# Performance work log

Hardware: AMD Instinct MI355X
Metric: run time of the kernel (lower is better)

## Reference

```python
import jax, jax.numpy as jnp
import numpy as np

NUM_GROUPS = 131072
GROUP_SIZE = 3          # trigenic interaction queries (Dango)
HIDDEN = 128
NUM_HEADS = 4
HEAD_DIM = HIDDEN // NUM_HEADS
NUM_LAYERS = 2


def setup_inputs() -> dict:
    key = jax.random.key(0)
    ks = jax.random.split(key, 16)
    N = NUM_GROUPS * GROUP_SIZE
    H, L = HIDDEN, NUM_LAYERS
    s = 1.0 / np.sqrt(H)
    inp = {
        "gene_embeddings": jax.random.normal(ks[0], (N, H), dtype=jnp.float32),
        "batch": jnp.repeat(jnp.arange(NUM_GROUPS, dtype=jnp.int64), GROUP_SIZE),
        # static embedding Linear
        "Ws": jax.random.uniform(ks[1], (H, H), jnp.float32, -s, s),
        "bs": jnp.zeros((H,), jnp.float32),
        # per-layer attention projections, stacked over layers
        "Wq": jax.random.uniform(ks[2], (L, H, H), jnp.float32, -s, s),
        "bq": jnp.zeros((L, H), jnp.float32),
        "Wk": jax.random.uniform(ks[3], (L, H, H), jnp.float32, -s, s),
        "bk": jnp.zeros((L, H), jnp.float32),
        "Wv": jax.random.uniform(ks[4], (L, H, H), jnp.float32, -s, s),
        "bv": jnp.zeros((L, H), jnp.float32),
        "Wo": jax.random.uniform(ks[5], (L, H, H), jnp.float32, -s, s),
        "bo": jnp.zeros((L, H), jnp.float32),
        # ReZero params, init 0.01 as in module
        "beta": jnp.full((L,), 0.01, jnp.float32),
        # prediction layer (xavier_uniform)
        "Wp": jax.random.uniform(ks[6], (H, 1), jnp.float32, -np.sqrt(6.0 / (H + 1)), np.sqrt(6.0 / (H + 1))),
        "bp": jnp.zeros((1,), jnp.float32),
    }
    return inp


def _attention_layer(xg, Wq, bq, Wk, bk, Wv, bv, Wo, bo, beta):
    # xg: [G, S, H] block-diagonal groups; exclude-self masked MHA + ReZero.
    G, S, H = xg.shape
    q = (xg @ Wq + bq).reshape(G, S, NUM_HEADS, HEAD_DIM)
    k = (xg @ Wk + bk).reshape(G, S, NUM_HEADS, HEAD_DIM)
    v = (xg @ Wv + bv).reshape(G, S, NUM_HEADS, HEAD_DIM)
    scores = jnp.einsum("gqhd,gkhd->ghqk", q, k) / np.sqrt(HEAD_DIM)
    self_mask = jnp.eye(S, dtype=bool)  # exclude self-attention
    scores = jnp.where(self_mask, -jnp.inf, scores)
    attn = jax.nn.softmax(scores, axis=-1)
    attn = jnp.nan_to_num(attn, nan=0.0)  # torch.nan_to_num parity
    out = jnp.einsum("ghqk,gkhd->gqhd", attn, v).reshape(G, S, H)
    out = out @ Wo + bo
    return xg + beta * out  # ReZero residual (dropout: eval mode identity)


def reference(gene_embeddings, batch, Ws, bs, Wq, bq, Wk, bk, Wv, bv, Wo, bo, beta, Wp, bp):
    N, H = gene_embeddings.shape
    G = N // GROUP_SIZE
    static = jax.nn.relu(gene_embeddings @ Ws + bs)  # static embedding MLP
    dyn = gene_embeddings.reshape(G, GROUP_SIZE, H)
    for i in range(NUM_LAYERS):
        dyn = _attention_layer(dyn, Wq[i], bq[i], Wk[i], bk[i],
                               Wv[i], bv[i], Wo[i], bo[i], beta[i])
    dyn = dyn.reshape(N, H)
    diff_sq = (dyn - static) ** 2
    gene_scores = (diff_sq @ Wp + bp).squeeze(-1)  # [N]
    # scatter_mean over batch ids
    sums = jax.ops.segment_sum(gene_scores, batch, num_segments=G)
    cnts = jax.ops.segment_sum(jnp.ones_like(gene_scores), batch, num_segments=G)
    interaction_scores = sums / jnp.maximum(cnts, 1.0)
    return interaction_scores[:, None]  # [G, 1]
```

## Files before the change

### kernel.cpp

```cpp
#include <hip/hip_runtime.h>

#define NGROUPS 131072
#define H 128
#define SG 3
#define NHEADS 4
#define HD 32
#define GB 16
#define MR 48
#define NT 512
#define BP 136
#define NLAYERS 2

typedef unsigned short u16;
typedef __bf16 bf16x8 __attribute__((ext_vector_type(8)));
typedef float floatx4 __attribute__((ext_vector_type(4)));

__device__ __forceinline__ float bf2f(u16 u) {
  union { unsigned int i; float f; } c; c.i = ((unsigned int)u) << 16; return c.f;
}
__device__ __forceinline__ u16 f2bf(float f) {
  union { float f; unsigned int i; } c; c.f = f;
  unsigned int x = c.i;
  x += 0x7fffu + ((x >> 16) & 1u);
  return (u16)(x >> 16);
}

__global__ void wconv_kernel(const float* __restrict__ Ws, const float* __restrict__ Wq,
                             const float* __restrict__ Wk, const float* __restrict__ Wv,
                             const float* __restrict__ Wo, u16* __restrict__ wt) {
  int idx = blockIdx.x * 256 + threadIdx.x;
  int slot = idx >> 14;
  int rem = idx & 16383;
  int n = rem >> 7, k = rem & 127;
  const float* src;
  if (slot == 0) src = Ws;
  else {
    int l = (slot - 1) >> 2, t = (slot - 1) & 3;
    const float* base = (t == 0) ? Wq : (t == 1) ? Wk : (t == 2) ? Wv : Wo;
    src = base + l * (H * H);
  }
  wt[idx] = f2bf(src[k * H + n]);
}

__device__ __forceinline__ void load_af(const u16* __restrict__ buf, int m0, int q8,
                                        bf16x8 af[3][4]) {
#pragma unroll
  for (int rt = 0; rt < 3; rt++)
#pragma unroll
    for (int kk = 0; kk < 4; kk++)
      af[rt][kk] = *reinterpret_cast<const bf16x8*>(buf + (rt * 16 + m0) * BP + kk * 32 + q8);
}

__device__ __forceinline__ void mm_sub(const bf16x8 af[3][4], const u16* __restrict__ W,
                                       int col, int q8, floatx4 acc[3]) {
  bf16x8 b[4];
#pragma unroll
  for (int kk = 0; kk < 4; kk++)
    b[kk] = *reinterpret_cast<const bf16x8*>(W + col * H + kk * 32 + q8);
#pragma unroll
  for (int rt = 0; rt < 3; rt++)
    acc[rt] = (floatx4){0.f, 0.f, 0.f, 0.f};
#pragma unroll
  for (int kk = 0; kk < 4; kk++)
#pragma unroll
    for (int rt = 0; rt < 3; rt++)
      acc[rt] = __builtin_amdgcn_mfma_f32_16x16x32_bf16(af[rt][kk], b[kk], acc[rt], 0, 0, 0);
}

__device__ __forceinline__ void store_bf(u16* __restrict__ buf, const floatx4 acc[3],
                                         float bias, int col, int qi) {
#pragma unroll
  for (int rt = 0; rt < 3; rt++)
#pragma unroll
    for (int r = 0; r < 4; r++)
      buf[(rt * 16 + qi * 4 + r) * BP + col] = f2bf(acc[rt][r] + bias);
}

__global__ void __launch_bounds__(NT, 4)
dango_kernel(const float* __restrict__ x, const u16* __restrict__ wt,
             const float* __restrict__ bs, const float* __restrict__ bq,
             const float* __restrict__ bk, const float* __restrict__ bv,
             const float* __restrict__ bo, const float* __restrict__ beta,
             const float* __restrict__ Wp, const float* __restrict__ bp,
             float* __restrict__ out)
{
  __shared__ u16 xbf[MR][BP];
  __shared__ u16 qbuf[MR][BP];
  __shared__ u16 kbuf[MR][BP];
  __shared__ float attnw[GB][NHEADS][SG][2];
  __shared__ float rowsc[MR][9];

  const int tid = threadIdx.x;
  const int lane = tid & 63;
  const int wave = tid >> 6;
  const int m0 = lane & 15;
  const int qi = lane >> 4;
  const int q8 = qi << 3;
  const int col = wave * 16 + m0;
  const int row0 = blockIdx.x * MR;

  float xdyn[3][4];
#pragma unroll
  for (int rt = 0; rt < 3; rt++)
#pragma unroll
    for (int r = 0; r < 4; r++) {
      int row = rt * 16 + qi * 4 + r;
      float v = x[(size_t)(row0 + row) * H + col];
      xdyn[rt][r] = v;
      xbf[row][col] = f2bf(v);
    }
  __syncthreads();

  float stat[3][4];
  bf16x8 af[3][4];
  floatx4 acc[3];

  load_af(&xbf[0][0], m0, q8, af);
  __syncthreads();

  mm_sub(af, wt, col, q8, acc);
  {
    float b = bs[col];
#pragma unroll
    for (int rt = 0; rt < 3; rt++)
#pragma unroll
      for (int r = 0; r < 4; r++)
        stat[rt][r] = fmaxf(acc[rt][r] + b, 0.f);
  }
  mm_sub(af, wt + (size_t)1 * H * H, col, q8, acc);
  store_bf(&qbuf[0][0], acc, bq[col], col, qi);
  mm_sub(af, wt + (size_t)2 * H * H, col, q8, acc);
  store_bf(&kbuf[0][0], acc, bk[col], col, qi);
  mm_sub(af, wt + (size_t)3 * H * H, col, q8, acc);
  store_bf(&xbf[0][0], acc, bv[col], col, qi);
  __syncthreads();

  for (int l = 0; l < NLAYERS; l++) {
    if (tid < GB * NHEADS * SG) {
      int g = tid / (NHEADS * SG);
      int rem = tid % (NHEADS * SG);
      int h = rem / SG;
      int i = rem % SG;
      int j0 = (i == 0) ? 1 : 0;
      int j1 = (i == 2) ? 1 : 2;
      const u16* qp = &qbuf[g * 3 + i][h * HD];
      const u16* k0p = &kbuf[g * 3 + j0][h * HD];
      const u16* k1p = &kbuf[g * 3 + j1][h * HD];
      float s0 = 0.f, s1 = 0.f;
#pragma unroll
      for (int d = 0; d < HD; d++) {
        float qv = bf2f(qp[d]);
        s0 += qv * bf2f(k0p[d]);
        s1 += qv * bf2f(k1p[d]);
      }
      s0 *= 0.17677669529663687f;
      s1 *= 0.17677669529663687f;
      float mx = fmaxf(s0, s1);
      float e0 = __expf(s0 - mx), e1 = __expf(s1 - mx);
      float inv = 1.f / (e0 + e1);
      attnw[g][h][i][0] = e0 * inv;
      attnw[g][h][i][1] = e1 * inv;
    }
    __syncthreads();

    for (int ch = tid; ch < MR * 16; ch += NT) {
      int r = ch >> 4, c0 = (ch & 15) << 3;
      int g = r / 3, i = r - g * 3, h = c0 >> 5;
      int j0 = (i == 0) ? 1 : 0;
      int j1 = (i == 2) ? 1 : 2;
      float a0 = attnw[g][h][i][0], a1 = attnw[g][h][i][1];
      const u16* v0 = &xbf[g * 3 + j0][c0];
      const u16* v1 = &xbf[g * 3 + j1][c0];
#pragma unroll
      for (int d = 0; d < 8; d++)
        qbuf[r][c0 + d] = f2bf(a0 * bf2f(v0[d]) + a1 * bf2f(v1[d]));
    }
    __syncthreads();

    const u16* wo = wt + (size_t)(1 + l * 4 + 3) * H * H;
    const float betal = beta[l];
    load_af(&qbuf[0][0], m0, q8, af);
    mm_sub(af, wo, col, q8, acc);
    {
      float b = bo[l * H + col];
#pragma unroll
      for (int rt = 0; rt < 3; rt++)
#pragma unroll
        for (int r = 0; r < 4; r++) {
          float nv = xdyn[rt][r] + betal * (acc[rt][r] + b);
          xdyn[rt][r] = nv;
          xbf[(rt * 16 + qi * 4 + r)][col] = f2bf(nv);
        }
    }
    __syncthreads();

    if (l + 1 < NLAYERS) {
      const u16* wq = wt + (size_t)(1 + (l + 1) * 4 + 0) * H * H;
      const u16* wk = wt + (size_t)(1 + (l + 1) * 4 + 1) * H * H;
      const u16* wv = wt + (size_t)(1 + (l + 1) * 4 + 2) * H * H;
      load_af(&xbf[0][0], m0, q8, af);
      __syncthreads();
      mm_sub(af, wq, col, q8, acc);
      store_bf(&qbuf[0][0], acc, bq[(l + 1) * H + col], col, qi);
      mm_sub(af, wk, col, q8, acc);
      store_bf(&kbuf[0][0], acc, bk[(l + 1) * H + col], col, qi);
      mm_sub(af, wv, col, q8, acc);
      store_bf(&xbf[0][0], acc, bv[(l + 1) * H + col], col, qi);
      __syncthreads();
    }
  }

  const float wpc = Wp[col];
  float rv[3][4];
#pragma unroll
  for (int rt = 0; rt < 3; rt++)
#pragma unroll
    for (int r = 0; r < 4; r++) {
      float d = xdyn[rt][r] - stat[rt][r];
      rv[rt][r] = d * d * wpc;
    }
#pragma unroll
  for (int mask = 1; mask <= 8; mask <<= 1)
#pragma unroll
    for (int rt = 0; rt < 3; rt++)
#pragma unroll
      for (int r = 0; r < 4; r++)
        rv[rt][r] += __shfl_xor(rv[rt][r], mask, 64);
  if (m0 == 0) {
#pragma unroll
    for (int rt = 0; rt < 3; rt++)
#pragma unroll
      for (int r = 0; r < 4; r++)
        rowsc[rt * 16 + qi * 4 + r][wave] = rv[rt][r];
  }
  __syncthreads();
  if (tid < GB) {
    const float bpv = bp[0];
    float s = 0.f;
#pragma unroll
    for (int i = 0; i < SG; i++) {
      int row = tid * 3 + i;
#pragma unroll
      for (int w = 0; w < 8; w++) s += rowsc[row][w];
    }
    out[blockIdx.x * GB + tid] = s * (1.f / 3.f) + bpv;
  }
}

extern "C" void kernel_launch(void* const* d_in, const int* in_sizes, int n_in,
                              void* d_out, int out_size, void* d_ws, size_t ws_size,
                              hipStream_t stream) {
  const float* x    = (const float*)d_in[0];
  const float* Ws   = (const float*)d_in[2];
  const float* bs   = (const float*)d_in[3];
  const float* Wq   = (const float*)d_in[4];
  const float* bq   = (const float*)d_in[5];
  const float* Wk   = (const float*)d_in[6];
  const float* bk   = (const float*)d_in[7];
  const float* Wv   = (const float*)d_in[8];
  const float* bv   = (const float*)d_in[9];
  const float* Wo   = (const float*)d_in[10];
  const float* bo   = (const float*)d_in[11];
  const float* beta = (const float*)d_in[12];
  const float* Wp   = (const float*)d_in[13];
  const float* bp   = (const float*)d_in[14];
  float* out = (float*)d_out;
  u16* wt = (u16*)d_ws;

  wconv_kernel<<<576, 256, 0, stream>>>(Ws, Wq, Wk, Wv, Wo, wt);
  dango_kernel<<<NGROUPS / GB, NT, 0, stream>>>(x, wt, bs, bq, bk, bv, bo, beta, Wp, bp, out);
}
```

Baseline: 616.8 us.

## Transpose MFMA operands so each lane owns four contiguous columns, vectorize LDS traffic

Swaps the A and B roles in the projection MFMAs so the weight tile is the A operand and the activations are B. Each lane now holds four consecutive output columns of one row, which allows float4 global loads of x, packed bf16x2 stores to LDS, and a shorter shuffle reduction at the end. The attention score and value-mix loops read and write LDS as uint4 instead of scalar u16. A separate V buffer removes one barrier, and the static branch is kept as packed bf16 to reduce register pressure under a fixed 4-waves-per-EU bound. The cost is extra LDS and a small precision loss in the static path.

```diff
diff --git a/kernel.cpp b/kernel.cpp
--- a/kernel.cpp
+++ b/kernel.cpp
@@ -1,4 +1,5 @@
 #include <hip/hip_runtime.h>
+#include <hip/hip_bf16.h>
 
 #define NGROUPS 131072
 #define H 128
@@ -12,16 +13,23 @@
 #define NLAYERS 2
 
 typedef unsigned short u16;
+typedef unsigned int u32;
 typedef __bf16 bf16x8 __attribute__((ext_vector_type(8)));
 typedef float floatx4 __attribute__((ext_vector_type(4)));
 
-__device__ __forceinline__ float bf2f(u16 u) {
-  union { unsigned int i; float f; } c; c.i = ((unsigned int)u) << 16; return c.f;
+__device__ __forceinline__ float bf2f_lo(u32 u) {
+  union { u32 i; float f; } c; c.i = u << 16; return c.f;
+}
+__device__ __forceinline__ float bf2f_hi(u32 u) {
+  union { u32 i; float f; } c; c.i = u & 0xffff0000u; return c.f;
+}
+__device__ __forceinline__ u32 f2bf2(float a, float b) {
+  __hip_bfloat162 h = __float22bfloat162_rn(make_float2(a, b));
+  union { __hip_bfloat162 h; u32 u; } c; c.h = h; return c.u;
 }
 __device__ __forceinline__ u16 f2bf(float f) {
-  union { float f; unsigned int i; } c; c.f = f;
-  unsigned int x = c.i;
-  x += 0x7fffu + ((x >> 16) & 1u);
+  union { float f; u32 i; } c; c.f = f;
+  u32 x = c.i; x += 0x7fffu + ((x >> 16) & 1u);
   return (u16)(x >> 16);
 }
 
@@ -42,41 +50,44 @@
   wt[idx] = f2bf(src[k * H + n]);
 }
 
-__device__ __forceinline__ void load_af(const u16* __restrict__ buf, int m0, int q8,
-                                        bf16x8 af[3][4]) {
-#pragma unroll
-  for (int rt = 0; rt < 3; rt++)
+__device__ __forceinline__ void load_bfrag(const u16* __restrict__ buf, int m0, int qi,
+                                           bf16x8 bf[3][4]) {
+#pragma unroll
+  for (int nt = 0; nt < 3; nt++)
 #pragma unroll
     for (int kk = 0; kk < 4; kk++)
-      af[rt][kk] = *reinterpret_cast<const bf16x8*>(buf + (rt * 16 + m0) * BP + kk * 32 + q8);
-}
-
-__device__ __forceinline__ void mm_sub(const bf16x8 af[3][4], const u16* __restrict__ W,
-                                       int col, int q8, floatx4 acc[3]) {
-  bf16x8 b[4];
+      bf[nt][kk] = *reinterpret_cast<const bf16x8*>(buf + (nt * 16 + m0) * BP + kk * 32 + qi * 8);
+}
+
+__device__ __forceinline__ void proj(const bf16x8 bf[3][4], const u16* __restrict__ W,
+                                     int wrow, int qi, floatx4 acc[3]) {
+  bf16x8 a[4];
 #pragma unroll
   for (int kk = 0; kk < 4; kk++)
-    b[kk] = *reinterpret_cast<const bf16x8*>(W + col * H + kk * 32 + q8);
-#pragma unroll
-  for (int rt = 0; rt < 3; rt++)
-    acc[rt] = (floatx4){0.f, 0.f, 0.f, 0.f};
+    a[kk] = *reinterpret_cast<const bf16x8*>(W + wrow * H + kk * 32 + qi * 8);
+#pragma unroll
+  for (int nt = 0; nt < 3; nt++)
+    acc[nt] = (floatx4){0.f, 0.f, 0.f, 0.f};
 #pragma unroll
   for (int kk = 0; kk < 4; kk++)
 #pragma unroll
-    for (int rt = 0; rt < 3; rt++)
-      acc[rt] = __builtin_amdgcn_mfma_f32_16x16x32_bf16(af[rt][kk], b[kk], acc[rt], 0, 0, 0);
-}
-
-__device__ __forceinline__ void store_bf(u16* __restrict__ buf, const floatx4 acc[3],
-                                         float bias, int col, int qi) {
-#pragma unroll
-  for (int rt = 0; rt < 3; rt++)
-#pragma unroll
-    for (int r = 0; r < 4; r++)
-      buf[(rt * 16 + qi * 4 + r) * BP + col] = f2bf(acc[rt][r] + bias);
-}
-
-__global__ void __launch_bounds__(NT, 4)
+    for (int nt = 0; nt < 3; nt++)
+      acc[nt] = __builtin_amdgcn_mfma_f32_16x16x32_bf16(a[kk], bf[nt][kk], acc[nt], 0, 0, 0);
+}
+
+__device__ __forceinline__ void store_proj(u16* __restrict__ buf, const floatx4 acc[3],
+                                           float4 b4, int m0, int colb) {
+#pragma unroll
+  for (int nt = 0; nt < 3; nt++) {
+    uint2 pp;
+    pp.x = f2bf2(acc[nt][0] + b4.x, acc[nt][1] + b4.y);
+    pp.y = f2bf2(acc[nt][2] + b4.z, acc[nt][3] + b4.w);
+    *reinterpret_cast<uint2*>(buf + (nt * 16 + m0) * BP + colb) = pp;
+  }
+}
+
+__global__ void __launch_bounds__(NT)
+__attribute__((amdgpu_waves_per_eu(4, 4)))
 dango_kernel(const float* __restrict__ x, const u16* __restrict__ wt,
              const float* __restrict__ bs, const float* __restrict__ bq,
              const float* __restrict__ bk, const float* __restrict__ bv,
@@ -84,9 +95,10 @@
              const float* __restrict__ Wp, const float* __restrict__ bp,
              float* __restrict__ out)
 {
-  __shared__ u16 xbf[MR][BP];
-  __shared__ u16 qbuf[MR][BP];
-  __shared__ u16 kbuf[MR][BP];
+  __shared__ __align__(16) u16 xbf[MR][BP];
+  __shared__ __align__(16) u16 qbuf[MR][BP];
+  __shared__ __align__(16) u16 kbuf[MR][BP];
+  __shared__ __align__(16) u16 vbuf[MR][BP];
   __shared__ float attnw[GB][NHEADS][SG][2];
   __shared__ float rowsc[MR][9];
 
@@ -95,44 +107,44 @@
   const int wave = tid >> 6;
   const int m0 = lane & 15;
   const int qi = lane >> 4;
-  const int q8 = qi << 3;
-  const int col = wave * 16 + m0;
+  const int colb = wave * 16 + qi * 4;
+  const int wrow = wave * 16 + m0;
   const int row0 = blockIdx.x * MR;
 
   float xdyn[3][4];
-#pragma unroll
-  for (int rt = 0; rt < 3; rt++)
-#pragma unroll
-    for (int r = 0; r < 4; r++) {
-      int row = rt * 16 + qi * 4 + r;
-      float v = x[(size_t)(row0 + row) * H + col];
-      xdyn[rt][r] = v;
-      xbf[row][col] = f2bf(v);
-    }
+  u32 statpk[3][2];
+
+#pragma unroll
+  for (int nt = 0; nt < 3; nt++) {
+    int row = nt * 16 + m0;
+    float4 v = *reinterpret_cast<const float4*>(x + (size_t)(row0 + row) * H + colb);
+    xdyn[nt][0] = v.x; xdyn[nt][1] = v.y; xdyn[nt][2] = v.z; xdyn[nt][3] = v.w;
+    uint2 pp; pp.x = f2bf2(v.x, v.y); pp.y = f2bf2(v.z, v.w);
+    *reinterpret_cast<uint2*>(&xbf[row][colb]) = pp;
+  }
   __syncthreads();
 
-  float stat[3][4];
-  bf16x8 af[3][4];
   floatx4 acc[3];
-
-  load_af(&xbf[0][0], m0, q8, af);
-  __syncthreads();
-
-  mm_sub(af, wt, col, q8, acc);
   {
-    float b = bs[col];
-#pragma unroll
-    for (int rt = 0; rt < 3; rt++)
-#pragma unroll
-      for (int r = 0; r < 4; r++)
-        stat[rt][r] = fmaxf(acc[rt][r] + b, 0.f);
-  }
-  mm_sub(af, wt + (size_t)1 * H * H, col, q8, acc);
-  store_bf(&qbuf[0][0], acc, bq[col], col, qi);
-  mm_sub(af, wt + (size_t)2 * H * H, col, q8, acc);
-  store_bf(&kbuf[0][0], acc, bk[col], col, qi);
-  mm_sub(af, wt + (size_t)3 * H * H, col, q8, acc);
-  store_bf(&xbf[0][0], acc, bv[col], col, qi);
+    bf16x8 bf[3][4];
+    load_bfrag(&xbf[0][0], m0, qi, bf);
+
+    proj(bf, wt, wrow, qi, acc);
+    {
+      float4 b4 = *reinterpret_cast<const float4*>(bs + colb);
+#pragma unroll
+      for (int nt = 0; nt < 3; nt++) {
+        statpk[nt][0] = f2bf2(fmaxf(acc[nt][0] + b4.x, 0.f), fmaxf(acc[nt][1] + b4.y, 0.f));
+        statpk[nt][1] = f2bf2(fmaxf(acc[nt][2] + b4.z, 0.f), fmaxf(acc[nt][3] + b4.w, 0.f));
+      }
+    }
+    proj(bf, wt + 1 * H * H, wrow, qi, acc);
+    store_proj(&qbuf[0][0], acc, *reinterpret_cast<const float4*>(bq + colb), m0, colb);
+    proj(bf, wt + 2 * H * H, wrow, qi, acc);
+    store_proj(&kbuf[0][0], acc, *reinterpret_cast<const float4*>(bk + colb), m0, colb);
+    proj(bf, wt + 3 * H * H, wrow, qi, acc);
+    store_proj(&vbuf[0][0], acc, *reinterpret_cast<const float4*>(bv + colb), m0, colb);
+  }
   __syncthreads();
 
   for (int l = 0; l < NLAYERS; l++) {
@@ -143,15 +155,22 @@
       int i = rem % SG;
       int j0 = (i == 0) ? 1 : 0;
       int j1 = (i == 2) ? 1 : 2;
-      const u16* qp = &qbuf[g * 3 + i][h * HD];
-      const u16* k0p = &kbuf[g * 3 + j0][h * HD];
-      const u16* k1p = &kbuf[g * 3 + j1][h * HD];
+      const uint4* qp  = reinterpret_cast<const uint4*>(&qbuf[g * 3 + i][h * HD]);
+      const uint4* k0p = reinterpret_cast<const uint4*>(&kbuf[g * 3 + j0][h * HD]);
+      const uint4* k1p = reinterpret_cast<const uint4*>(&kbuf[g * 3 + j1][h * HD]);
       float s0 = 0.f, s1 = 0.f;
 #pragma unroll
-      for (int d = 0; d < HD; d++) {
-        float qv = bf2f(qp[d]);
-        s0 += qv * bf2f(k0p[d]);
-        s1 += qv * bf2f(k1p[d]);
+      for (int c = 0; c < 4; c++) {
+        uint4 qu = qp[c], u0 = k0p[c], u1 = k1p[c];
+        u32 qs[4] = {qu.x, qu.y, qu.z, qu.w};
+        u32 a0[4] = {u0.x, u0.y, u0.z, u0.w};
+        u32 a1[4] = {u1.x, u1.y, u1.z, u1.w};
+#pragma unroll
+        for (int e = 0; e < 4; e++) {
+          float ql = bf2f_lo(qs[e]), qh = bf2f_hi(qs[e]);
+          s0 += ql * bf2f_lo(a0[e]) + qh * bf2f_hi(a0[e]);
+          s1 += ql * bf2f_lo(a1[e]) + qh * bf2f_hi(a1[e]);
+        }
       }
       s0 *= 0.17677669529663687f;
       s1 *= 0.17677669529663687f;
@@ -169,73 +188,81 @@
       int j0 = (i == 0) ? 1 : 0;
       int j1 = (i == 2) ? 1 : 2;
       float a0 = attnw[g][h][i][0], a1 = attnw[g][h][i][1];
-      const u16* v0 = &xbf[g * 3 + j0][c0];
-      const u16* v1 = &xbf[g * 3 + j1][c0];
-#pragma unroll
-      for (int d = 0; d < 8; d++)
-        qbuf[r][c0 + d] = f2bf(a0 * bf2f(v0[d]) + a1 * bf2f(v1[d]));
+      uint4 v0 = *reinterpret_cast<const uint4*>(&vbuf[g * 3 + j0][c0]);
+      uint4 v1 = *reinterpret_cast<const uint4*>(&vbuf[g * 3 + j1][c0]);
+      u32 w0[4] = {v0.x, v0.y, v0.z, v0.w};
+      u32 w1[4] = {v1.x, v1.y, v1.z, v1.w};
+      u32 oo[4];
+#pragma unroll
+      for (int e = 0; e < 4; e++) {
+        float lo = a0 * bf2f_lo(w0[e]) + a1 * bf2f_lo(w1[e]);
+        float hi = a0 * bf2f_hi(w0[e]) + a1 * bf2f_hi(w1[e]);
+        oo[e] = f2bf2(lo, hi);
+      }
+      uint4 o; o.x = oo[0]; o.y = oo[1]; o.z = oo[2]; o.w = oo[3];
+      *reinterpret_cast<uint4*>(&qbuf[r][c0]) = o;
     }
     __syncthreads();
 
-    const u16* wo = wt + (size_t)(1 + l * 4 + 3) * H * H;
-    const float betal = beta[l];
-    load_af(&qbuf[0][0], m0, q8, af);
-    mm_sub(af, wo, col, q8, acc);
     {
-      float b = bo[l * H + col];
-#pragma unroll
-      for (int rt = 0; rt < 3; rt++)
-#pragma unroll
-        for (int r = 0; r < 4; r++) {
-          float nv = xdyn[rt][r] + betal * (acc[rt][r] + b);
-          xdyn[rt][r] = nv;
-          xbf[(rt * 16 + qi * 4 + r)][col] = f2bf(nv);
-        }
-    }
-    __syncthreads();
+      bf16x8 bf[3][4];
+      load_bfrag(&qbuf[0][0], m0, qi, bf);
+      proj(bf, wt + (size_t)(1 + l * 4 + 3) * H * H, wrow, qi, acc);
+      float4 b4 = *reinterpret_cast<const float4*>(bo + l * H + colb);
+      const float betal = beta[l];
+#pragma unroll
+      for (int nt = 0; nt < 3; nt++) {
+        xdyn[nt][0] += betal * (acc[nt][0] + b4.x);
+        xdyn[nt][1] += betal * (acc[nt][1] + b4.y);
+        xdyn[nt][2] += betal * (acc[nt][2] + b4.z);
+        xdyn[nt][3] += betal * (acc[nt][3] + b4.w);
+      }
+    }
 
     if (l + 1 < NLAYERS) {
-      const u16* wq = wt + (size_t)(1 + (l + 1) * 4 + 0) * H * H;
-      const u16* wk = wt + (size_t)(1 + (l + 1) * 4 + 1) * H * H;
-      const u16* wv = wt + (size_t)(1 + (l + 1) * 4 + 2) * H * H;
-      load_af(&xbf[0][0], m0, q8, af);
+#pragma unroll
+      for (int nt = 0; nt < 3; nt++) {
+        uint2 pp;
+        pp.x = f2bf2(xdyn[nt][0], xdyn[nt][1]);
+        pp.y = f2bf2(xdyn[nt][2], xdyn[nt][3]);
+        *reinterpret_cast<uint2*>(&xbf[nt * 16 + m0][colb]) = pp;
+      }
       __syncthreads();
-      mm_sub(af, wq, col, q8, acc);
-      store_bf(&qbuf[0][0], acc, bq[(l + 1) * H + col], col, qi);
-      mm_sub(af, wk, col, q8, acc);
-      store_bf(&kbuf[0][0], acc, bk[(l + 1) * H + col], col, qi);
-      mm_sub(af, wv, col, q8, acc);
-      store_bf(&xbf[0][0], acc, bv[(l + 1) * H + col], col, qi);
+
+      bf16x8 bf[3][4];
+      load_bfrag(&xbf[0][0], m0, qi, bf);
+      proj(bf, wt + (size_t)(1 + (l + 1) * 4 + 0) * H * H, wrow, qi, acc);
+      store_proj(&qbuf[0][0], acc, *reinterpret_cast<const float4*>(bq + (l + 1) * H + colb), m0, colb);
+      proj(bf, wt + (size_t)(1 + (l + 1) * 4 + 1) * H * H, wrow, qi, acc);
+      store_proj(&kbuf[0][0], acc, *reinterpret_cast<const float4*>(bk + (l + 1) * H + colb), m0, colb);
+      proj(bf, wt + (size_t)(1 + (l + 1) * 4 + 2) * H * H, wrow, qi, acc);
+      store_proj(&vbuf[0][0], acc, *reinterpret_cast<const float4*>(bv + (l + 1) * H + colb), m0, colb);
       __syncthreads();
     }
   }
 
-  const float wpc = Wp[col];
-  float rv[3][4];
-#pragma unroll
-  for (int rt = 0; rt < 3; rt++)
-#pragma unroll
-    for (int r = 0; r < 4; r++) {
-      float d = xdyn[rt][r] - stat[rt][r];
-      rv[rt][r] = d * d * wpc;
-    }
-#pragma unroll
-  for (int mask = 1; mask <= 8; mask <<= 1)
-#pragma unroll
-    for (int rt = 0; rt < 3; rt++)
-#pragma unroll
-      for (int r = 0; r < 4; r++)
-        rv[rt][r] += __shfl_xor(rv[rt][r], mask, 64);
-  if (m0 == 0) {
-#pragma unroll
-    for (int rt = 0; rt < 3; rt++)
-#pragma unroll
-      for (int r = 0; r < 4; r++)
-        rowsc[rt * 16 + qi * 4 + r][wave] = rv[rt][r];
+  float4 wp4 = *reinterpret_cast<const float4*>(Wp + colb);
+  float rsum[3];
+#pragma unroll
+  for (int nt = 0; nt < 3; nt++) {
+    float d0 = xdyn[nt][0] - bf2f_lo(statpk[nt][0]);
+    float d1 = xdyn[nt][1] - bf2f_hi(statpk[nt][0]);
+    float d2 = xdyn[nt][2] - bf2f_lo(statpk[nt][1]);
+    float d3 = xdyn[nt][3] - bf2f_hi(statpk[nt][1]);
+    rsum[nt] = d0 * d0 * wp4.x + d1 * d1 * wp4.y + d2 * d2 * wp4.z + d3 * d3 * wp4.w;
+  }
+#pragma unroll
+  for (int nt = 0; nt < 3; nt++) {
+    rsum[nt] += __shfl_xor(rsum[nt], 16, 64);
+    rsum[nt] += __shfl_xor(rsum[nt], 32, 64);
+  }
+  if (qi == 0) {
+#pragma unroll
+    for (int nt = 0; nt < 3; nt++)
+      rowsc[nt * 16 + m0][wave] = rsum[nt];
   }
   __syncthreads();
   if (tid < GB) {
-    const float bpv = bp[0];
     float s = 0.f;
 #pragma unroll
     for (int i = 0; i < SG; i++) {
@@ -243,7 +270,7 @@
 #pragma unroll
       for (int w = 0; w < 8; w++) s += rowsc[row][w];
     }
-    out[blockIdx.x * GB + tid] = s * (1.f / 3.f) + bpv;
+    out[blockIdx.x * GB + tid] = s * (1.f / 3.f) + bp[0];
   }
 }
 
```

Result: no change. 609.3 us (-1.2%).
